# Optimization experiments

Measured on AMD Instinct MI355X. Metric: run time of the kernel, lower is better.

The kernel has to match this reference:

```python
import jax, jax.numpy as jnp
import numpy as np

B, D, H = 16384, 1024, 1024


def setup_inputs() -> dict:
    key = jax.random.key(0)
    ks = jax.random.split(key, 6)
    s = 1.0 / np.sqrt(D)
    return {
        "x": jax.random.normal(ks[0], (B, D), jnp.float32),
        "h_prev": jax.random.normal(ks[1], (B, H), jnp.float32),
        "c_prev": jax.random.normal(ks[2], (B, H), jnp.float32),
        "dynamic_weight": jax.random.uniform(ks[3], (B, H), jnp.float32),
        # stacked gate weights: order [i, f, o, c, s] along first axis
        "Wx": jax.random.normal(ks[4], (5 * H, D), jnp.float32) * s,
        "bx": jnp.zeros((5 * H,), jnp.float32),
        "Uh": jax.random.normal(ks[5], (5 * H, H), jnp.float32) * s,
        "bh": jnp.zeros((5 * H,), jnp.float32),
    }


def reference(x, h_prev, c_prev, dynamic_weight, Wx, bx, Uh, bh):
    # two fused GEMMs covering all 10 original nn.Linear calls
    gates = (jnp.einsum('bd,gd->bg', x, Wx) + bx
             + jnp.einsum('bh,gh->bg', h_prev, Uh) + bh)  # [B, 5H]
    gi, gf, go, gc, gs = jnp.split(gates, 5, axis=-1)
    i_t = jax.nn.sigmoid(gi)
    f_t = jax.nn.sigmoid(gf)
    o_t = jax.nn.sigmoid(go)
    c_hat = jnp.tanh(gc)
    s_t = jax.nn.sigmoid(gs) * dynamic_weight
    c_t = f_t * c_prev + i_t * c_hat * s_t
    h_t = o_t * jnp.tanh(c_t)
    return h_t, c_t
```

## Files before the change

### kernel.cpp

```cpp
#include <hip/hip_runtime.h>
#include <hip/hip_bf16.h>

#define B_ROWS 16384
#define KDIM   2048
#define NDIM   5120
#define HDIM   1024

#define BM 256
#define BN 320
#define BK 64
#define NKT (KDIM / BK)
#define A_BYTES (BM * BK * 2)
#define W_BYTES (BN * BK * 2)
#define BUFSZ   (A_BYTES + W_BYTES)
#define LDS_BYTES (2 * BUFSZ)

typedef __attribute__((ext_vector_type(8))) short short8;
typedef __attribute__((ext_vector_type(4))) float f32x4;

__device__ __forceinline__ void async_cp16(const void* g, void* l) {
  __builtin_amdgcn_global_load_lds(
      (const __attribute__((address_space(1))) void*)g,
      (__attribute__((address_space(3))) void*)l,
      16, 0, 0);
}

__global__ void detect_dtype(const unsigned short* __restrict__ p, int* flag) {
  __shared__ int cnt;
  if (threadIdx.x == 0) cnt = 0;
  __syncthreads();
  int h = 0;
  for (int i = threadIdx.x; i < 2048; i += 256) {
    int e = (p[i] >> 7) & 0xFF;
    if (e >= 137) h++;
  }
  atomicAdd(&cnt, h);
  __syncthreads();
  if (threadIdx.x == 0) *flag = (cnt >= 4) ? 1 : 0;
}

__global__ void pack_pair_f32(const float* __restrict__ s0, const float* __restrict__ s1,
                              __hip_bfloat16* __restrict__ dst, const int* __restrict__ flag,
                              long rbase, long total) {
  if (*flag == 0) return;
  long idx = ((long)blockIdx.x * blockDim.x + threadIdx.x) * 8;
  if (idx >= total) return;
  int  k = (int)(idx & (KDIM - 1));
  long r = (idx >> 11) + rbase;
  const float* s = (k < 1024) ? (s0 + r * 1024 + k) : (s1 + r * 1024 + (k - 1024));
  float4 v0 = ((const float4*)s)[0];
  float4 v1 = ((const float4*)s)[1];
  union { short8 v; __hip_bfloat16 e[8]; } u;
  u.e[0] = __float2bfloat16(v0.x); u.e[1] = __float2bfloat16(v0.y);
  u.e[2] = __float2bfloat16(v0.z); u.e[3] = __float2bfloat16(v0.w);
  u.e[4] = __float2bfloat16(v1.x); u.e[5] = __float2bfloat16(v1.y);
  u.e[6] = __float2bfloat16(v1.z); u.e[7] = __float2bfloat16(v1.w);
  *(short8*)(dst + idx) = u.v;
}

__global__ __launch_bounds__(512, 2) void gemm_fused(
    const __hip_bfloat16* __restrict__ Abf, const __hip_bfloat16* __restrict__ Wbf,
    const void* __restrict__ xr, const void* __restrict__ hr,
    const void* __restrict__ Wxr, const void* __restrict__ Uhr,
    const void* __restrict__ cpr, const void* __restrict__ dwr,
    const void* __restrict__ bxr, const void* __restrict__ bhr,
    float* __restrict__ out, const int* __restrict__ flag, int row_base) {
  extern __shared__ char lds[];

  const int tid = threadIdx.x;
  const int w   = tid >> 6;
  const int l   = tid & 63;

  const int m0l = blockIdx.y * BM;
  const int h0  = blockIdx.x * 64;

  const int wm = w >> 2;
  const int wn = w & 3;

  const int fl = *flag;
  const int dc = (l & 7) ^ (l >> 3);

  const __hip_bfloat16* srcA;
  long strA, dA;
  if (fl) {
    srcA = Abf + (long)(m0l + w * 8 + (l >> 3)) * KDIM + dc * 8;
    strA = KDIM; dA = 1024;
  } else {
    srcA = (const __hip_bfloat16*)xr
         + (long)(row_base + m0l + w * 8 + (l >> 3)) * 1024 + dc * 8;
    strA = 1024;
    dA = (const __hip_bfloat16*)hr - (const __hip_bfloat16*)xr;
  }

  const __hip_bfloat16* srcW[5];
  long dW;
  {
    const __hip_bfloat16* wbase;
    long strW;
    if (fl) { wbase = Wbf; strW = KDIM; dW = 1024; }
    else {
      wbase = (const __hip_bfloat16*)Wxr; strW = 1024;
      dW = (const __hip_bfloat16*)Uhr - (const __hip_bfloat16*)Wxr;
    }
#pragma unroll
    for (int i = 0; i < 5; ++i) {
      const int j  = w + i * 8;
      const int wg = j / 10;
      const int q  = j % 10;
      const int g  = q >> 1;
      const int hs = (q & 1) * 8 + (l >> 3);
      const long r_w = (long)g * 1024 + h0 + wg * 16 + hs;
      srcW[i] = wbase + r_w * strW + dc * 8;
    }
  }

#define STAGE(T) do {                                                        \
    const int  b_  = (T) & 1;                                                \
    const int  k0_ = (T) * BK;                                               \
    const long koA_ = (k0_ < 1024) ? (long)k0_ : (dA + (k0_ - 1024));        \
    const long koW_ = (k0_ < 1024) ? (long)k0_ : (dW + (k0_ - 1024));        \
    char* lb_ = lds + b_ * BUFSZ;                                            \
    _Pragma("unroll")                                                        \
    for (int i_ = 0; i_ < 4; ++i_)                                           \
      async_cp16(srcA + koA_ + (long)i_ * 64 * strA,                         \
                 lb_ + (w + i_ * 8) * 1024 + l * 16);                        \
    _Pragma("unroll")                                                        \
    for (int i_ = 0; i_ < 5; ++i_)                                           \
      async_cp16(srcW[i_] + koW_,                                            \
                 lb_ + A_BYTES + (w + i_ * 8) * 1024 + l * 16);              \
  } while (0)

  f32x4 acc[8][5] = {};
  const int frow = l & 15;
  const int aoff0 = (wm * 128 + frow) * 128;
  const int woff0 = A_BYTES + (wn * 80 + frow) * 128;

#define COMPUTE(T) do {                                                      \
    const char* ba_ = lds + ((T) & 1) * BUFSZ;                               \
    _Pragma("unroll")                                                        \
    for (int kk = 0; kk < 2; ++kk) {                                         \
      const int sc_ = ((kk * 4 + (l >> 4)) ^ (l & 7)) * 16;                  \
      short8 wf_[5], af_[8];                                                 \
      _Pragma("unroll")                                                      \
      for (int nj = 0; nj < 5; ++nj)                                         \
        wf_[nj] = *(const short8*)(ba_ + woff0 + nj * 2048 + sc_);           \
      _Pragma("unroll")                                                      \
      for (int mi = 0; mi < 8; ++mi)                                         \
        af_[mi] = *(const short8*)(ba_ + aoff0 + mi * 2048 + sc_);           \
      __builtin_amdgcn_s_setprio(1);                                         \
      _Pragma("unroll")                                                      \
      for (int mi = 0; mi < 8; ++mi)                                         \
        _Pragma("unroll")                                                    \
        for (int nj = 0; nj < 5; ++nj)                                       \
          acc[mi][nj] = __builtin_amdgcn_mfma_f32_16x16x32_bf16(             \
              af_[mi], wf_[nj], acc[mi][nj], 0, 0, 0);                       \
      __builtin_amdgcn_s_setprio(0);                                         \
    }                                                                        \
  } while (0)

  STAGE(0);

  for (int t = 0; t < NKT - 1; ++t) {
    __builtin_amdgcn_s_barrier();
    __builtin_amdgcn_sched_barrier(0);
    STAGE(t + 1);
    asm volatile("s_waitcnt vmcnt(9)" ::: "memory");
    __builtin_amdgcn_sched_barrier(0);
    __builtin_amdgcn_s_barrier();
    __builtin_amdgcn_sched_barrier(0);
    COMPUTE(t);
  }
  __builtin_amdgcn_s_barrier();
  asm volatile("s_waitcnt vmcnt(0)" ::: "memory");
  __builtin_amdgcn_sched_barrier(0);
  __builtin_amdgcn_s_barrier();
  __builtin_amdgcn_sched_barrier(0);
  COMPUTE(NKT - 1);

#undef STAGE
#undef COMPUTE

  const int hh = h0 + wn * 16 + frow;
  float bsum[5];
#pragma unroll
  for (int g = 0; g < 5; ++g) {
    if (fl) {
      bsum[g] = ((const float*)bxr)[g * 1024 + hh] + ((const float*)bhr)[g * 1024 + hh];
    } else {
      bsum[g] = __bfloat162float(((const __hip_bfloat16*)bxr)[g * 1024 + hh])
              + __bfloat162float(((const __hip_bfloat16*)bhr)[g * 1024 + hh]);
    }
  }
  const long orow0 = (long)row_base + m0l + wm * 128 + (l >> 4) * 4;
  float* outc = out + (long)B_ROWS * HDIM;
#pragma unroll
  for (int mi = 0; mi < 8; ++mi) {
#pragma unroll
    for (int r = 0; r < 4; ++r) {
      const long idx = (orow0 + mi * 16 + r) * HDIM + hh;
      float cp, dv;
      if (fl) {
        cp = ((const float*)cpr)[idx];
        dv = ((const float*)dwr)[idx];
      } else {
        cp = __bfloat162float(((const __hip_bfloat16*)cpr)[idx]);
        dv = __bfloat162float(((const __hip_bfloat16*)dwr)[idx]);
      }
      const float gi = acc[mi][0][r] + bsum[0];
      const float gf = acc[mi][1][r] + bsum[1];
      const float go = acc[mi][2][r] + bsum[2];
      const float gc = acc[mi][3][r] + bsum[3];
      const float gs = acc[mi][4][r] + bsum[4];
      const float it = 1.f / (1.f + __expf(-gi));
      const float ft = 1.f / (1.f + __expf(-gf));
      const float ot = 1.f / (1.f + __expf(-go));
      const float ch = tanhf(gc);
      const float st = (1.f / (1.f + __expf(-gs))) * dv;
      const float ct = ft * cp + it * ch * st;
      out[idx]  = ot * tanhf(ct);
      outc[idx] = ct;
    }
  }
}

extern "C" void kernel_launch(void* const* d_in, const int* in_sizes, int n_in,
                              void* d_out, int out_size, void* d_ws, size_t ws_size,
                              hipStream_t stream) {
  const void* x      = d_in[0];
  const void* h_prev = d_in[1];
  const void* c_prev = d_in[2];
  const void* dw     = d_in[3];
  const void* Wx     = d_in[4];
  const void* bx     = d_in[5];
  const void* Uh     = d_in[6];
  const void* bh     = d_in[7];

  static int lds_attr_done = 0;
  if (!lds_attr_done) {
    hipFuncSetAttribute((const void*)gemm_fused,
                        hipFuncAttributeMaxDynamicSharedMemorySize, LDS_BYTES);
    lds_attr_done = 1;
  }

  const size_t wbf_bytes = (size_t)NDIM * KDIM * 2;
  int nc = 32;
  for (int c = 1; c <= 32; c <<= 1) {
    size_t need = 256 + wbf_bytes
                + (size_t)(B_ROWS / c) * KDIM * 2;
    if (need <= ws_size) { nc = c; break; }
  }
  const long rows = B_ROWS / nc;

  char* ws = (char*)d_ws;
  int* flag = (int*)ws;
  __hip_bfloat16* Wbf = (__hip_bfloat16*)(ws + 256);
  __hip_bfloat16* Abf = (__hip_bfloat16*)(ws + 256 + wbf_bytes);

  detect_dtype<<<1, 256, 0, stream>>>((const unsigned short*)x, flag);

  pack_pair_f32<<<(int)(((long)NDIM * KDIM) / 2048), 256, 0, stream>>>(
      (const float*)Wx, (const float*)Uh, Wbf, flag, 0, (long)NDIM * KDIM);

  for (int c = 0; c < nc; ++c) {
    long rbase = c * rows;
    pack_pair_f32<<<(int)rows, 256, 0, stream>>>(
        (const float*)x, (const float*)h_prev, Abf, flag, rbase, rows * KDIM);
    dim3 grid(NDIM / BN, (int)(rows / BM));
    gemm_fused<<<grid, 512, LDS_BYTES, stream>>>(
        Abf, Wbf, x, h_prev, Wx, Uh, c_prev, dw, bx, bh,
        (float*)d_out, flag, (int)rbase);
  }
}
```

Measured before the change: 681.6 us.

## Deepen GEMM pipeline to 4 stages with BK=32 and XCD-aware block swizzle

Halves the K tile to 32 and uses four LDS buffers so three tiles are in flight at once, with the vmcnt waits adjusted to match. Load assignment is rewritten with a new LDS swizzle for 64-byte rows, and the grid becomes 1D with a remap that spreads consecutive blocks across the 8 XCDs for better L2 reuse. The aim is to hide global-load latency and improve cache locality, at the cost of twice as many barriers per K and uneven load counts across waves.

```diff
diff --git a/kernel.cpp b/kernel.cpp
--- a/kernel.cpp
+++ b/kernel.cpp
@@ -8,12 +8,13 @@
 
 #define BM 256
 #define BN 320
-#define BK 64
+#define BK 32
 #define NKT (KDIM / BK)
 #define A_BYTES (BM * BK * 2)
 #define W_BYTES (BN * BK * 2)
 #define BUFSZ   (A_BYTES + W_BYTES)
-#define LDS_BYTES (2 * BUFSZ)
+#define NBUF  4
+#define LDS_BYTES (NBUF * BUFSZ)
 
 typedef __attribute__((ext_vector_type(8))) short short8;
 typedef __attribute__((ext_vector_type(4))) float f32x4;
@@ -71,28 +72,38 @@
   const int w   = tid >> 6;
   const int l   = tid & 63;
 
-  const int m0l = blockIdx.y * BM;
-  const int h0  = blockIdx.x * 64;
+  const int nb  = gridDim.x;
+  const int q8  = nb >> 3;
+  const int sw  = (blockIdx.x & 7) * q8 + (blockIdx.x >> 3);
+  const int m0l = (sw >> 4) * BM;
+  const int h0  = (sw & 15) * 64;
 
   const int wm = w >> 2;
   const int wn = w & 3;
 
   const int fl = *flag;
-  const int dc = (l & 7) ^ (l >> 3);
-
-  const __hip_bfloat16* srcA;
-  long strA, dA;
-  if (fl) {
-    srcA = Abf + (long)(m0l + w * 8 + (l >> 3)) * KDIM + dc * 8;
-    strA = KDIM; dA = 1024;
-  } else {
-    srcA = (const __hip_bfloat16*)xr
-         + (long)(row_base + m0l + w * 8 + (l >> 3)) * 1024 + dc * 8;
-    strA = 1024;
-    dA = (const __hip_bfloat16*)hr - (const __hip_bfloat16*)xr;
-  }
-
-  const __hip_bfloat16* srcW[5];
+  const int dc = (l & 3) ^ ((l >> 3) & 3);
+
+  const __hip_bfloat16 *srcA0, *srcA1;
+  long dA;
+  {
+    const int r0 = m0l + w * 32 + (l >> 2);
+    if (fl) {
+      srcA0 = Abf + (long)r0 * KDIM + dc * 8;
+      srcA1 = Abf + (long)(r0 + 16) * KDIM + dc * 8;
+      dA = 1024;
+    } else {
+      srcA0 = (const __hip_bfloat16*)xr + (long)(row_base + r0) * 1024 + dc * 8;
+      srcA1 = (const __hip_bfloat16*)xr + (long)(row_base + r0 + 16) * 1024 + dc * 8;
+      dA = (const __hip_bfloat16*)hr - (const __hip_bfloat16*)xr;
+    }
+  }
+
+  const bool has3 = (w < 4);
+  const int  jw0  = has3 ? (3 * w)     : (2 * w + 4);
+  const int  jw1  = has3 ? (3 * w + 1) : (2 * w + 5);
+  const int  jw2  = has3 ? (3 * w + 2) : (2 * w + 5);
+  const __hip_bfloat16 *srcW0, *srcW1, *srcW2;
   long dW;
   {
     const __hip_bfloat16* wbase;
@@ -102,80 +113,74 @@
       wbase = (const __hip_bfloat16*)Wxr; strW = 1024;
       dW = (const __hip_bfloat16*)Uhr - (const __hip_bfloat16*)Wxr;
     }
-#pragma unroll
-    for (int i = 0; i < 5; ++i) {
-      const int j  = w + i * 8;
-      const int wg = j / 10;
-      const int q  = j % 10;
-      const int g  = q >> 1;
-      const int hs = (q & 1) * 8 + (l >> 3);
-      const long r_w = (long)g * 1024 + h0 + wg * 16 + hs;
-      srcW[i] = wbase + r_w * strW + dc * 8;
-    }
+    const int j0g = jw0 % 5, j0w = jw0 / 5;
+    const int j1g = jw1 % 5, j1w = jw1 / 5;
+    const int j2g = jw2 % 5, j2w = jw2 / 5;
+    srcW0 = wbase + ((long)j0g * 1024 + h0 + j0w * 16 + (l >> 2)) * strW + dc * 8;
+    srcW1 = wbase + ((long)j1g * 1024 + h0 + j1w * 16 + (l >> 2)) * strW + dc * 8;
+    srcW2 = wbase + ((long)j2g * 1024 + h0 + j2w * 16 + (l >> 2)) * strW + dc * 8;
   }
 
 #define STAGE(T) do {                                                        \
-    const int  b_  = (T) & 1;                                                \
+    const int  b_  = (T) & 3;                                                \
     const int  k0_ = (T) * BK;                                               \
     const long koA_ = (k0_ < 1024) ? (long)k0_ : (dA + (k0_ - 1024));        \
     const long koW_ = (k0_ < 1024) ? (long)k0_ : (dW + (k0_ - 1024));        \
     char* lb_ = lds + b_ * BUFSZ;                                            \
+    async_cp16(srcA0 + koA_, lb_ + w * 2048 + l * 16);                       \
+    async_cp16(srcA1 + koA_, lb_ + w * 2048 + 1024 + l * 16);                \
+    async_cp16(srcW0 + koW_, lb_ + A_BYTES + jw0 * 1024 + l * 16);           \
+    async_cp16(srcW1 + koW_, lb_ + A_BYTES + jw1 * 1024 + l * 16);           \
+    if (has3)                                                                \
+      async_cp16(srcW2 + koW_, lb_ + A_BYTES + jw2 * 1024 + l * 16);         \
+  } while (0)
+
+  f32x4 acc[8][5] = {};
+  const int frow  = l & 15;
+  const int swz   = ((l >> 4) ^ ((frow >> 1) & 3)) << 4;
+  const int aoff0 = (wm * 128 + frow) * 64;
+  const int woff0 = A_BYTES + (wn * 80 + frow) * 64;
+
+#define COMPUTE(T) do {                                                      \
+    const char* ba_ = lds + ((T) & 3) * BUFSZ;                               \
+    short8 af_[8], wf_[5];                                                   \
     _Pragma("unroll")                                                        \
-    for (int i_ = 0; i_ < 4; ++i_)                                           \
-      async_cp16(srcA + koA_ + (long)i_ * 64 * strA,                         \
-                 lb_ + (w + i_ * 8) * 1024 + l * 16);                        \
+    for (int nj = 0; nj < 5; ++nj)                                           \
+      wf_[nj] = *(const short8*)(ba_ + woff0 + nj * 1024 + swz);             \
     _Pragma("unroll")                                                        \
-    for (int i_ = 0; i_ < 5; ++i_)                                           \
-      async_cp16(srcW[i_] + koW_,                                            \
-                 lb_ + A_BYTES + (w + i_ * 8) * 1024 + l * 16);              \
-  } while (0)
-
-  f32x4 acc[8][5] = {};
-  const int frow = l & 15;
-  const int aoff0 = (wm * 128 + frow) * 128;
-  const int woff0 = A_BYTES + (wn * 80 + frow) * 128;
-
-#define COMPUTE(T) do {                                                      \
-    const char* ba_ = lds + ((T) & 1) * BUFSZ;                               \
+    for (int mi = 0; mi < 8; ++mi)                                           \
+      af_[mi] = *(const short8*)(ba_ + aoff0 + mi * 1024 + swz);             \
+    __builtin_amdgcn_s_setprio(1);                                           \
     _Pragma("unroll")                                                        \
-    for (int kk = 0; kk < 2; ++kk) {                                         \
-      const int sc_ = ((kk * 4 + (l >> 4)) ^ (l & 7)) * 16;                  \
-      short8 wf_[5], af_[8];                                                 \
+    for (int mi = 0; mi < 8; ++mi)                                           \
       _Pragma("unroll")                                                      \
       for (int nj = 0; nj < 5; ++nj)                                         \
-        wf_[nj] = *(const short8*)(ba_ + woff0 + nj * 2048 + sc_);           \
-      _Pragma("unroll")                                                      \
-      for (int mi = 0; mi < 8; ++mi)                                         \
-        af_[mi] = *(const short8*)(ba_ + aoff0 + mi * 2048 + sc_);           \
-      __builtin_amdgcn_s_setprio(1);                                         \
-      _Pragma("unroll")                                                      \
-      for (int mi = 0; mi < 8; ++mi)                                         \
-        _Pragma("unroll")                                                    \
-        for (int nj = 0; nj < 5; ++nj)                                       \
-          acc[mi][nj] = __builtin_amdgcn_mfma_f32_16x16x32_bf16(             \
-              af_[mi], wf_[nj], acc[mi][nj], 0, 0, 0);                       \
-      __builtin_amdgcn_s_setprio(0);                                         \
-    }                                                                        \
+        acc[mi][nj] = __builtin_amdgcn_mfma_f32_16x16x32_bf16(               \
+            af_[mi], wf_[nj], acc[mi][nj], 0, 0, 0);                         \
+    __builtin_amdgcn_s_setprio(0);                                           \
   } while (0)
 
-  STAGE(0);
-
-  for (int t = 0; t < NKT - 1; ++t) {
-    __builtin_amdgcn_s_barrier();
-    __builtin_amdgcn_sched_barrier(0);
-    STAGE(t + 1);
-    asm volatile("s_waitcnt vmcnt(9)" ::: "memory");
+  STAGE(0); STAGE(1); STAGE(2);
+
+  for (int t = 0; t < NKT - 3; ++t) {
+    __builtin_amdgcn_s_barrier();
+    __builtin_amdgcn_sched_barrier(0);
+    STAGE(t + 3);
+    if (has3) { asm volatile("s_waitcnt vmcnt(15)" ::: "memory"); }
+    else      { asm volatile("s_waitcnt vmcnt(12)" ::: "memory"); }
     __builtin_amdgcn_sched_barrier(0);
     __builtin_amdgcn_s_barrier();
     __builtin_amdgcn_sched_barrier(0);
     COMPUTE(t);
   }
-  __builtin_amdgcn_s_barrier();
-  asm volatile("s_waitcnt vmcnt(0)" ::: "memory");
-  __builtin_amdgcn_sched_barrier(0);
-  __builtin_amdgcn_s_barrier();
-  __builtin_amdgcn_sched_barrier(0);
-  COMPUTE(NKT - 1);
+  for (int t = NKT - 3; t < NKT; ++t) {
+    __builtin_amdgcn_s_barrier();
+    asm volatile("s_waitcnt vmcnt(0)" ::: "memory");
+    __builtin_amdgcn_sched_barrier(0);
+    __builtin_amdgcn_s_barrier();
+    __builtin_amdgcn_sched_barrier(0);
+    COMPUTE(t);
+  }
 
 #undef STAGE
 #undef COMPUTE
@@ -265,8 +270,8 @@
     long rbase = c * rows;
     pack_pair_f32<<<(int)rows, 256, 0, stream>>>(
         (const float*)x, (const float*)h_prev, Abf, flag, rbase, rows * KDIM);
-    dim3 grid(NDIM / BN, (int)(rows / BM));
-    gemm_fused<<<grid, 512, LDS_BYTES, stream>>>(
+    const int nblocks = (int)(16 * (rows / BM));
+    gemm_fused<<<nblocks, 512, LDS_BYTES, stream>>>(
         Abf, Wbf, x, h_prev, Wx, Uh, c_prev, dw, bx, bh,
         (float*)d_out, flag, (int)rbase);
   }
```

Result: slower. 706.9 us (+3.7%).
